# Kernel tuning notes

Hardware: AMD Instinct MI355X
Metric: run time of the kernel (lower is better)

Reference implementation:

```python
import jax, jax.numpy as jnp
import numpy as np
from jax import lax

B, N, T, H = 128, 2, 256, 128  # batch, inc_nodes, seq_len, lstm hidden


def setup_inputs() -> dict:
    key = jax.random.key(0)
    ks = jax.random.split(key, 20)
    r = lambda i, shape, s: (jax.random.normal(ks[i], shape) * s).astype(jnp.float32)
    return {
        "x": r(0, (B, N, T), 1.0),
        "h0": r(1, (N, 4, B, H), 1.0),   # (node, layer*D+dir, B, H), torch.randn init states
        "c0": r(2, (N, 4, B, H), 1.0),
        "w_ih0": r(3, (N, 2, 4 * H, 1), 0.05),
        "w_hh0": r(4, (N, 2, 4 * H, H), 0.05),
        "b0": r(5, (N, 2, 4 * H), 0.05),
        "w_ih1": r(6, (N, 2, 4 * H, 2 * H), 0.05),
        "w_hh1": r(7, (N, 2, 4 * H, H), 0.05),
        "b1": r(8, (N, 2, 4 * H), 0.05),
        "w_fc0": r(9, (N * 2 * H, 256), 0.05), "b_fc0": r(10, (256,), 0.05),
        "ln0_a": r(11, (256,), 1.0), "ln0_b": r(12, (256,), 1.0),
        "w_fc1": r(13, (256, 256), 0.05), "b_fc1": r(14, (256,), 0.05),
        "ln1_a": r(15, (256,), 1.0), "ln1_b": r(16, (256,), 1.0),
        "w_fc2": r(17, (256, 64), 0.05), "b_fc2": r(18, (64,), 0.05),
    }


def _lstm_dir(xp, h0, c0, w_hh):
    # xp: [T, B, 4H] precomputed input projections + bias; returns [T, B, H]
    def step(hc, xt):
        h, c = hc
        g = xt + h @ w_hh.T
        i, f, gg, o = jnp.split(g, 4, axis=-1)  # torch gate order i,f,g,o
        c = jax.nn.sigmoid(f) * c + jax.nn.sigmoid(i) * jnp.tanh(gg)
        h = jax.nn.sigmoid(o) * jnp.tanh(c)
        return (h, c), h
    _, hs = lax.scan(step, (h0, c0), xp)
    return hs


def _bidir(x, h0, c0, w_ih, w_hh, b):
    # x: [B,T,Din]; h0,c0: [2,B,H]; w_ih: [2,4H,Din]; w_hh: [2,4H,H]; b: [2,4H]
    xp_f = jnp.moveaxis(x @ w_ih[0].T + b[0], 1, 0)            # [T,B,4H]
    hf = _lstm_dir(xp_f, h0[0], c0[0], w_hh[0])
    xp_b = jnp.moveaxis(x[:, ::-1] @ w_ih[1].T + b[1], 1, 0)
    hb = _lstm_dir(xp_b, h0[1], c0[1], w_hh[1])[::-1]
    return jnp.moveaxis(jnp.concatenate([hf, hb], axis=-1), 0, 1)  # [B,T,2H]


def _node(xn, h0n, c0n, wi0, wh0, bb0, wi1, wh1, bb1):
    # xn: [B,T,1]; h0n/c0n: [4,B,H] laid out (l0f, l0b, l1f, l1b)
    y = _bidir(xn, h0n[0:2], c0n[0:2], wi0, wh0, bb0)
    y = _bidir(y, h0n[2:4], c0n[2:4], wi1, wh1, bb1)
    return y[:, -1]  # last timestep, [B,2H]


def _layernorm(x, a, b, eps=1e-6):
    mu = jnp.mean(x, axis=-1, keepdims=True)
    std = jnp.std(x, axis=-1, keepdims=True, ddof=1) + eps  # torch.std is unbiased
    return (x - mu) / std * a + b


def reference(x, h0, c0, w_ih0, w_hh0, b0, w_ih1, w_hh1, b1,
              w_fc0, b_fc0, ln0_a, ln0_b, w_fc1, b_fc1, ln1_a, ln1_b, w_fc2, b_fc2):
    bsz = x.shape[0]
    xs = jnp.moveaxis(x, 1, 0)[..., None]  # [N,B,T,1]
    outs = jax.vmap(_node)(xs, h0, c0, w_ih0, w_hh0, b0, w_ih1, w_hh1, b1)  # [N,B,2H]
    t = jnp.moveaxis(outs, 0, 1).reshape(bsz, -1)  # hstack over nodes -> [B, N*2H]
    t = t @ w_fc0 + b_fc0
    t = jax.nn.relu(t + _layernorm(t, ln0_a, ln0_b))
    t = t @ w_fc1 + b_fc1
    t = jax.nn.relu(t + _layernorm(t, ln1_a, ln1_b))
    t = t @ w_fc2 + b_fc2
    return t.reshape(-1, 1, t.shape[-1])  # [B,1,out_dim]
```

## Files before the change

kernel.cpp:

```cpp
#include <hip/hip_runtime.h>
#include <hip/hip_fp16.h>

#define T_SEQ 256

typedef _Float16 half8 __attribute__((ext_vector_type(8)));
typedef float float4v __attribute__((ext_vector_type(4)));

__device__ __forceinline__ float fexp2(float x) { return __builtin_amdgcn_exp2f(x); }
__device__ __forceinline__ float frcp(float x) { return __builtin_amdgcn_rcpf(x); }
__device__ __forceinline__ float sigf(float x) { return frcp(1.f + fexp2(-1.4426950408889634f * x)); }
__device__ __forceinline__ float tanhf_(float x) { return 1.f - 2.f * frcp(1.f + fexp2(2.8853900817779268f * x)); }

__device__ __forceinline__ void gload_lds16(const void* g, void* l) {
    __builtin_amdgcn_global_load_lds((const __attribute__((address_space(1))) void*)g,
                                     (__attribute__((address_space(3))) void*)l, 16, 0, 0);
}

__device__ __forceinline__ void relaxed_barrier() {
    __builtin_amdgcn_sched_barrier(0);
    asm volatile("s_waitcnt lgkmcnt(0)" ::: "memory");
    __builtin_amdgcn_s_barrier();
    asm volatile("" ::: "memory");
    __builtin_amdgcn_sched_barrier(0);
}
__device__ __forceinline__ void vm_barrier() {
    __builtin_amdgcn_sched_barrier(0);
    asm volatile("s_waitcnt vmcnt(0) lgkmcnt(0)" ::: "memory");
    __builtin_amdgcn_s_barrier();
    asm volatile("" ::: "memory");
    __builtin_amdgcn_sched_barrier(0);
}

__global__ __launch_bounds__(512, 1) void lstm_l0(
    const float* __restrict__ x, const float* __restrict__ h0,
    const float* __restrict__ c0, const float* __restrict__ wih0,
    const float* __restrict__ whh0, const float* __restrict__ b0,
    _Float16* __restrict__ y0f) {
    const int wg = blockIdx.x;
    const int chain = wg >> 3, n = chain >> 1, d = chain & 1;
    const int bg = wg & 7, bbase = bg * 16;
    const int tid = threadIdx.x;
    const int wave = tid >> 6, lane = tid & 63, lrow = lane & 15, lgrp = lane >> 4;

    __shared__ __align__(16) float xsT[T_SEQ][16];
    __shared__ __align__(16) _Float16 hfrag[2][4][64][8];

    {
        int r = tid >> 5, ck = tid & 31;
        const float* xr = &x[((bbase + r) * 2 + n) * T_SEQ + ck * 8];
        float4v v0 = *(const float4v*)xr, v1 = *(const float4v*)(xr + 4);
#pragma unroll
        for (int i = 0; i < 4; ++i) { xsT[ck * 8 + i][r] = v0[i]; xsT[ck * 8 + 4 + i][r] = v1[i]; }
    }
    const int sidx = n * 4 + d;
    for (int idx = tid; idx < 256; idx += 512) {
        int kk = idx >> 6, l = idx & 63;
        int b = bbase + (l & 15), k0 = kk * 32 + (l >> 4) * 8;
        const float4v* s4 = (const float4v*)&h0[((size_t)(sidx * 128 + b)) * 128 + k0];
        float4v v0 = s4[0], v1 = s4[1];
        _Float16* dp = &hfrag[0][kk][l][0];
#pragma unroll
        for (int j = 0; j < 4; ++j) { dp[j] = (_Float16)v0[j]; dp[4 + j] = (_Float16)v1[j]; }
    }
    float wi[4], bi[4];
    half8 wf[4][4];
#pragma unroll
    for (int p = 0; p < 4; ++p) {
        int g = (wave + 8 * p) * 16 + lrow;
        wi[p] = wih0[chain * 512 + g];
        bi[p] = b0[chain * 512 + g];
        const float* sg = &whh0[(size_t)(chain * 512 + g) * 128];
#pragma unroll
        for (int kk = 0; kk < 4; ++kk) {
            const float4v* s4 = (const float4v*)&sg[kk * 32 + lgrp * 8];
            float4v v0 = s4[0], v1 = s4[1];
            half8 h;
#pragma unroll
            for (int j = 0; j < 4; ++j) { h[j] = (_Float16)v0[j]; h[4 + j] = (_Float16)v1[j]; }
            wf[p][kk] = h;
        }
    }
    const int hc = wave * 16 + lrow;
    float creg[4];
#pragma unroll
    for (int jj = 0; jj < 4; ++jj)
        creg[jj] = c0[((size_t)(sidx * 128 + bbase + 4 * lgrp + jj)) * 128 + hc];
    __syncthreads();

    const int kkw = hc >> 5, lsub = (hc >> 3) & 3, jd = hc & 7;

    for (int t = 0; t < T_SEQ; ++t) {
        const int cur = t & 1, nxt = cur ^ 1;
        const int tx = d ? (T_SEQ - 1 - t) : t;
        half8 a[4];
#pragma unroll
        for (int kk = 0; kk < 4; ++kk) a[kk] = *(const half8*)&hfrag[cur][kk][lane][0];
        if (t > 0 && tid < 256) {
            const int txp = d ? (T_SEQ - t) : (t - 1);
            half8 v = ((const half8*)&hfrag[cur][0][0][0])[tid];
            half8* dst = (half8*)&y0f[((size_t)(n * 256 + txp) * 8 + bg) * 4096 + d * 2048];
            dst[tid] = v;
        }
        float4v xv = *(const float4v*)&xsT[tx][4 * lgrp];
        float4v acc[4];
#pragma unroll
        for (int p = 0; p < 4; ++p) {
#pragma unroll
            for (int jj = 0; jj < 4; ++jj) acc[p][jj] = fmaf(xv[jj], wi[p], bi[p]);
        }
#pragma unroll
        for (int kk = 0; kk < 4; ++kk)
#pragma unroll
            for (int p = 0; p < 4; ++p)
                acc[p] = __builtin_amdgcn_mfma_f32_16x16x32_f16(a[kk], wf[p][kk], acc[p], 0, 0, 0);
#pragma unroll
        for (int jj = 0; jj < 4; ++jj) {
            float ig = sigf(acc[0][jj]), fg = sigf(acc[1][jj]);
            float gg = tanhf_(acc[2][jj]), og = sigf(acc[3][jj]);
            float c = fmaf(fg, creg[jj], ig * gg);
            creg[jj] = c;
            hfrag[nxt][kkw][16 * lsub + 4 * lgrp + jj][jd] = (_Float16)(og * tanhf_(c));
        }
        relaxed_barrier();
    }
    if (tid < 256) {
        const int txl = d ? 0 : (T_SEQ - 1);
        half8 v = ((const half8*)&hfrag[0][0][0][0])[tid];
        half8* dst = (half8*)&y0f[((size_t)(n * 256 + txl) * 8 + bg) * 4096 + d * 2048];
        dst[tid] = v;
    }
}

__global__ __launch_bounds__(512, 1) void lstm_l1(
    const float* __restrict__ h0, const float* __restrict__ c0,
    const float* __restrict__ wih1, const float* __restrict__ whh1,
    const float* __restrict__ b1, const _Float16* __restrict__ y0f,
    float* __restrict__ lo) {
    const int wg = blockIdx.x;
    const int chain = wg >> 3, n = chain >> 1, d = chain & 1;
    const int bg = wg & 7, bbase = bg * 16;
    const int tid = threadIdx.x;
    const int wave = tid >> 6, lane = tid & 63, lrow = lane & 15, lgrp = lane >> 4;

    __shared__ __align__(16) _Float16 ybuf[2][4096];
    __shared__ __align__(16) _Float16 hfrag[2][4][64][8];

    const int sidx = n * 4 + 2 + d;
    for (int idx = tid; idx < 256; idx += 512) {
        int kk = idx >> 6, l = idx & 63;
        int b = bbase + (l & 15), k0 = kk * 32 + (l >> 4) * 8;
        const float4v* s4 = (const float4v*)&h0[((size_t)(sidx * 128 + b)) * 128 + k0];
        float4v v0 = s4[0], v1 = s4[1];
        _Float16* dp = &hfrag[0][kk][l][0];
#pragma unroll
        for (int j = 0; j < 4; ++j) { dp[j] = (_Float16)v0[j]; dp[4 + j] = (_Float16)v1[j]; }
    }
    float bi[4];
    half8 wih[4][8];
    half8 wf[4][4];
#pragma unroll
    for (int p = 0; p < 4; ++p) {
        int g = (wave + 8 * p) * 16 + lrow;
        bi[p] = b1[chain * 512 + g];
        const float* sg = &wih1[(size_t)(chain * 512 + g) * 256];
#pragma unroll
        for (int kk = 0; kk < 8; ++kk) {
            const float4v* s4 = (const float4v*)&sg[kk * 32 + lgrp * 8];
            float4v v0 = s4[0], v1 = s4[1];
            half8 h;
#pragma unroll
            for (int j = 0; j < 4; ++j) { h[j] = (_Float16)v0[j]; h[4 + j] = (_Float16)v1[j]; }
            wih[p][kk] = h;
        }
        const float* sh = &whh1[(size_t)(chain * 512 + g) * 128];
#pragma unroll
        for (int kk = 0; kk < 4; ++kk) {
            const float4v* s4 = (const float4v*)&sh[kk * 32 + lgrp * 8];
            float4v v0 = s4[0], v1 = s4[1];
            half8 h;
#pragma unroll
            for (int j = 0; j < 4; ++j) { h[j] = (_Float16)v0[j]; h[4 + j] = (_Float16)v1[j]; }
            wf[p][kk] = h;
        }
    }
    const int hc = wave * 16 + lrow;
    float creg[4];
#pragma unroll
    for (int jj = 0; jj < 4; ++jj)
        creg[jj] = c0[((size_t)(sidx * 128 + bbase + 4 * lgrp + jj)) * 128 + hc];

    const int nsteps = d ? 1 : T_SEQ;
    const int t0 = d ? (T_SEQ - 1) : 0;
    gload_lds16(&y0f[(((size_t)n * 256 + t0) * 8 + bg) * 4096 + (size_t)tid * 8],
                &ybuf[0][wave * 512]);
    asm volatile("s_waitcnt vmcnt(0)" ::: "memory");
    __syncthreads();

    const int kkw = hc >> 5, lsub = (hc >> 3) & 3, jd = hc & 7;

    for (int t = 0; t < nsteps; ++t) {
        const int cur = t & 1, nxt = cur ^ 1;
        if (t + 1 < nsteps)
            gload_lds16(&y0f[(((size_t)n * 256 + (t + 1)) * 8 + bg) * 4096 + (size_t)tid * 8],
                        &ybuf[nxt][wave * 512]);
        half8 ay[8], ah[4];
#pragma unroll
        for (int kk = 0; kk < 8; ++kk) ay[kk] = *(const half8*)&ybuf[cur][kk * 512 + lane * 8];
#pragma unroll
        for (int kk = 0; kk < 4; ++kk) ah[kk] = *(const half8*)&hfrag[cur][kk][lane][0];
        float4v acc[4];
#pragma unroll
        for (int p = 0; p < 4; ++p) acc[p] = (float4v){bi[p], bi[p], bi[p], bi[p]};
#pragma unroll
        for (int kk = 0; kk < 8; ++kk)
#pragma unroll
            for (int p = 0; p < 4; ++p)
                acc[p] = __builtin_amdgcn_mfma_f32_16x16x32_f16(ay[kk], wih[p][kk], acc[p], 0, 0, 0);
#pragma unroll
        for (int kk = 0; kk < 4; ++kk)
#pragma unroll
            for (int p = 0; p < 4; ++p)
                acc[p] = __builtin_amdgcn_mfma_f32_16x16x32_f16(ah[kk], wf[p][kk], acc[p], 0, 0, 0);
        float hout[4];
#pragma unroll
        for (int jj = 0; jj < 4; ++jj) {
            float ig = sigf(acc[0][jj]), fg = sigf(acc[1][jj]);
            float gg = tanhf_(acc[2][jj]), og = sigf(acc[3][jj]);
            float c = fmaf(fg, creg[jj], ig * gg);
            creg[jj] = c;
            hout[jj] = og * tanhf_(c);
        }
#pragma unroll
        for (int jj = 0; jj < 4; ++jj)
            hfrag[nxt][kkw][16 * lsub + 4 * lgrp + jj][jd] = (_Float16)hout[jj];
        if (t == nsteps - 1) {
#pragma unroll
            for (int jj = 0; jj < 4; ++jj)
                lo[(size_t)(bbase + 4 * lgrp + jj) * 512 + n * 256 + d * 128 + hc] = hout[jj];
        }
        vm_barrier();
    }
}

__global__ __launch_bounds__(256) void head_k(
    const float* __restrict__ lo,
    const float* __restrict__ w0, const float* __restrict__ bb0,
    const float* __restrict__ a0, const float* __restrict__ g0,
    const float* __restrict__ w1, const float* __restrict__ bb1,
    const float* __restrict__ a1, const float* __restrict__ g1,
    const float* __restrict__ w2, const float* __restrict__ bb2,
    float* __restrict__ out) {
    const int b = blockIdx.x, j = threadIdx.x;
    const int lane = j & 63, wid = j >> 6;
    __shared__ float row[512];
    __shared__ float buf[256];
    __shared__ float redA[4], redB[4];

    row[j] = lo[b * 512 + j];
    row[256 + j] = lo[b * 512 + 256 + j];
    __syncthreads();

    float s = bb0[j];
#pragma unroll 8
    for (int k = 0; k < 512; ++k) s = fmaf(row[k], w0[k * 256 + j], s);
    float v = s, v2 = s * s;
#pragma unroll
    for (int off = 32; off; off >>= 1) { v += __shfl_xor(v, off); v2 += __shfl_xor(v2, off); }
    if (lane == 0) { redA[wid] = v; redB[wid] = v2; }
    __syncthreads();
    float S = redA[0] + redA[1] + redA[2] + redA[3];
    float SS = redB[0] + redB[1] + redB[2] + redB[3];
    float mu = S * (1.f / 256.f);
    float var = (SS - S * mu) * (1.f / 255.f);
    float stdv = sqrtf(var) + 1e-6f;
    float t0 = fmaxf(s + (s - mu) / stdv * a0[j] + g0[j], 0.f);
    buf[j] = t0;
    __syncthreads();

    float s1 = bb1[j];
#pragma unroll 8
    for (int k = 0; k < 256; ++k) s1 = fmaf(buf[k], w1[k * 256 + j], s1);
    v = s1; v2 = s1 * s1;
#pragma unroll
    for (int off = 32; off; off >>= 1) { v += __shfl_xor(v, off); v2 += __shfl_xor(v2, off); }
    if (lane == 0) { redA[wid] = v; redB[wid] = v2; }
    __syncthreads();
    S = redA[0] + redA[1] + redA[2] + redA[3];
    SS = redB[0] + redB[1] + redB[2] + redB[3];
    mu = S * (1.f / 256.f);
    var = (SS - S * mu) * (1.f / 255.f);
    stdv = sqrtf(var) + 1e-6f;
    float t1 = fmaxf(s1 + (s1 - mu) / stdv * a1[j] + g1[j], 0.f);
    __syncthreads();
    buf[j] = t1;
    __syncthreads();

    if (j < 64) {
        float s2 = bb2[j];
#pragma unroll 8
        for (int k = 0; k < 256; ++k) s2 = fmaf(buf[k], w2[k * 64 + j], s2);
        out[b * 64 + j] = s2;
    }
}

extern "C" void kernel_launch(void* const* d_in, const int* in_sizes, int n_in,
                              void* d_out, int out_size, void* d_ws, size_t ws_size,
                              hipStream_t stream) {
    const float* x    = (const float*)d_in[0];
    const float* h0   = (const float*)d_in[1];
    const float* c0   = (const float*)d_in[2];
    const float* wih0 = (const float*)d_in[3];
    const float* whh0 = (const float*)d_in[4];
    const float* bb0  = (const float*)d_in[5];
    const float* wih1 = (const float*)d_in[6];
    const float* whh1 = (const float*)d_in[7];
    const float* bb1  = (const float*)d_in[8];
    const float* wfc0 = (const float*)d_in[9];
    const float* bfc0 = (const float*)d_in[10];
    const float* ln0a = (const float*)d_in[11];
    const float* ln0b = (const float*)d_in[12];
    const float* wfc1 = (const float*)d_in[13];
    const float* bfc1 = (const float*)d_in[14];
    const float* ln1a = (const float*)d_in[15];
    const float* ln1b = (const float*)d_in[16];
    const float* wfc2 = (const float*)d_in[17];
    const float* bfc2 = (const float*)d_in[18];

    char* ws = (char*)d_ws;
    _Float16* y0f = (_Float16*)ws;
    float*    lo  = (float*)(ws + (size_t)33554432);

    lstm_l0<<<dim3(32), dim3(512), 0, stream>>>(x, h0, c0, wih0, whh0, bb0, y0f);
    lstm_l1<<<dim3(32), dim3(512), 0, stream>>>(h0, c0, wih1, whh1, bb1, y0f, lo);
    head_k<<<dim3(128), dim3(256), 0, stream>>>(lo, wfc0, bfc0, ln0a, ln0b,
                                                wfc1, bfc1, ln1a, ln1b, wfc2, bfc2,
                                                (float*)d_out);
}
```

Measured before the change: 755.9 us.

## Split LSTM batch across four times more workgroups with 4-row tiles

Each LSTM chain now runs on 32 workgroups of 4 batch rows instead of 8 workgroups of 16 rows, so 128 workgroups are launched in place of 32 and more compute units stay busy on the serial recurrence. MFMA tiles keep a 16-row shape, but only 4 rows are real and the rest are zero-padded. Gate values are redistributed through an LDS bounce buffer so each lane handles one element, and the MFMA accumulation is split into independent chains to shorten dependency latency. Each step pays for a wasted share of MFMA work and an extra LDS round trip.

Result: slower. 910.9 us (+20.5%).

```diff
diff --git a/kernel.cpp b/kernel.cpp
--- a/kernel.cpp
+++ b/kernel.cpp
@@ -5,6 +5,7 @@
 
 typedef _Float16 half8 __attribute__((ext_vector_type(8)));
 typedef float float4v __attribute__((ext_vector_type(4)));
+typedef float float2v __attribute__((ext_vector_type(2)));
 
 __device__ __forceinline__ float fexp2(float x) { return __builtin_amdgcn_exp2f(x); }
 __device__ __forceinline__ float frcp(float x) { return __builtin_amdgcn_rcpf(x); }
@@ -37,28 +38,29 @@
     const float* __restrict__ whh0, const float* __restrict__ b0,
     _Float16* __restrict__ y0f) {
     const int wg = blockIdx.x;
-    const int chain = wg >> 3, n = chain >> 1, d = chain & 1;
-    const int bg = wg & 7, bbase = bg * 16;
+    const int chain = wg >> 5, n = chain >> 1, d = chain & 1;
+    const int bg4 = wg & 31, bg16 = bg4 >> 2, ro0 = (bg4 & 3) * 4, bbase = bg4 * 4;
     const int tid = threadIdx.x;
     const int wave = tid >> 6, lane = tid & 63, lrow = lane & 15, lgrp = lane >> 4;
 
-    __shared__ __align__(16) float xsT[T_SEQ][16];
+    __shared__ __align__(16) float xsT[T_SEQ][4];
     __shared__ __align__(16) _Float16 hfrag[2][4][64][8];
-
+    __shared__ __align__(16) float bounce[8][4][4][64];
+
+    ((float4v*)hfrag)[tid] = (float4v){0.f, 0.f, 0.f, 0.f};
     {
-        int r = tid >> 5, ck = tid & 31;
-        const float* xr = &x[((bbase + r) * 2 + n) * T_SEQ + ck * 8];
-        float4v v0 = *(const float4v*)xr, v1 = *(const float4v*)(xr + 4);
-#pragma unroll
-        for (int i = 0; i < 4; ++i) { xsT[ck * 8 + i][r] = v0[i]; xsT[ck * 8 + 4 + i][r] = v1[i]; }
-    }
+        int r = tid >> 7, c2 = (tid & 127) * 2;
+        float2v v = *(const float2v*)&x[((bbase + r) * 2 + n) * T_SEQ + c2];
+        xsT[c2][r] = v[0];
+        xsT[c2 + 1][r] = v[1];
+    }
+    __syncthreads();
     const int sidx = n * 4 + d;
-    for (int idx = tid; idx < 256; idx += 512) {
-        int kk = idx >> 6, l = idx & 63;
-        int b = bbase + (l & 15), k0 = kk * 32 + (l >> 4) * 8;
-        const float4v* s4 = (const float4v*)&h0[((size_t)(sidx * 128 + b)) * 128 + k0];
+    if (tid < 64) {
+        int kk = tid >> 4, q = (tid >> 2) & 3, r = tid & 3;
+        const float4v* s4 = (const float4v*)&h0[((size_t)(sidx * 128 + bbase + r)) * 128 + kk * 32 + q * 8];
         float4v v0 = s4[0], v1 = s4[1];
-        _Float16* dp = &hfrag[0][kk][l][0];
+        _Float16* dp = &hfrag[0][kk][16 * q + r][0];
 #pragma unroll
         for (int j = 0; j < 4; ++j) { dp[j] = (_Float16)v0[j]; dp[4 + j] = (_Float16)v1[j]; }
     }
@@ -81,13 +83,11 @@
         }
     }
     const int hc = wave * 16 + lrow;
-    float creg[4];
-#pragma unroll
-    for (int jj = 0; jj < 4; ++jj)
-        creg[jj] = c0[((size_t)(sidx * 128 + bbase + 4 * lgrp + jj)) * 128 + hc];
-    __syncthreads();
-
-    const int kkw = hc >> 5, lsub = (hc >> 3) & 3, jd = hc & 7;
+    float creg = c0[((size_t)(sidx * 128 + bbase + lgrp)) * 128 + hc];
+    __syncthreads();
+
+    const int kkw = hc >> 5, lw = 16 * ((hc >> 3) & 3), jw = hc & 7;
+    const int wb = wave * 8 + lane;
 
     for (int t = 0; t < T_SEQ; ++t) {
         const int cur = t & 1, nxt = cur ^ 1;
@@ -95,39 +95,49 @@
         half8 a[4];
 #pragma unroll
         for (int kk = 0; kk < 4; ++kk) a[kk] = *(const half8*)&hfrag[cur][kk][lane][0];
-        if (t > 0 && tid < 256) {
+        if (t > 0 && lane < 8) {
             const int txp = d ? (T_SEQ - t) : (t - 1);
-            half8 v = ((const half8*)&hfrag[cur][0][0][0])[tid];
-            half8* dst = (half8*)&y0f[((size_t)(n * 256 + txp) * 8 + bg) * 4096 + d * 2048];
-            dst[tid] = v;
-        }
-        float4v xv = *(const float4v*)&xsT[tx][4 * lgrp];
-        float4v acc[4];
-#pragma unroll
-        for (int p = 0; p < 4; ++p) {
-#pragma unroll
-            for (int jj = 0; jj < 4; ++jj) acc[p][jj] = fmaf(xv[jj], wi[p], bi[p]);
-        }
-#pragma unroll
-        for (int kk = 0; kk < 4; ++kk)
-#pragma unroll
-            for (int p = 0; p < 4; ++p)
-                acc[p] = __builtin_amdgcn_mfma_f32_16x16x32_f16(a[kk], wf[p][kk], acc[p], 0, 0, 0);
-#pragma unroll
-        for (int jj = 0; jj < 4; ++jj) {
-            float ig = sigf(acc[0][jj]), fg = sigf(acc[1][jj]);
-            float gg = tanhf_(acc[2][jj]), og = sigf(acc[3][jj]);
-            float c = fmaf(fg, creg[jj], ig * gg);
-            creg[jj] = c;
-            hfrag[nxt][kkw][16 * lsub + 4 * lgrp + jj][jd] = (_Float16)(og * tanhf_(c));
-        }
+            const int kkh = wb >> 4, q = (wb >> 2) & 3, ro = wb & 3;
+            half8 v = *(const half8*)&hfrag[cur][kkh][16 * q + ro][0];
+            *(half8*)&y0f[((size_t)(n * 256 + txp) * 8 + bg16) * 4096 +
+                          (size_t)((d * 4 + kkh) * 64 + 16 * q + ro0 + ro) * 8] = v;
+        }
+        float4v xv = *(const float4v*)&xsT[tx][0];
+        float4v accA[4], accB[4];
+#pragma unroll
+        for (int p = 0; p < 4; ++p) {
+#pragma unroll
+            for (int jj = 0; jj < 4; ++jj) accA[p][jj] = fmaf(xv[jj], wi[p], bi[p]);
+            accB[p] = (float4v){0.f, 0.f, 0.f, 0.f};
+        }
+#pragma unroll
+        for (int p = 0; p < 4; ++p) {
+            accA[p] = __builtin_amdgcn_mfma_f32_16x16x32_f16(a[0], wf[p][0], accA[p], 0, 0, 0);
+            accA[p] = __builtin_amdgcn_mfma_f32_16x16x32_f16(a[1], wf[p][1], accA[p], 0, 0, 0);
+            accB[p] = __builtin_amdgcn_mfma_f32_16x16x32_f16(a[2], wf[p][2], accB[p], 0, 0, 0);
+            accB[p] = __builtin_amdgcn_mfma_f32_16x16x32_f16(a[3], wf[p][3], accB[p], 0, 0, 0);
+        }
+#pragma unroll
+        for (int p = 0; p < 4; ++p) {
+            float4v g = accA[p] + accB[p];
+            *(float4v*)&bounce[wave][p][lgrp][lrow * 4] = g;
+        }
+        float gate[4];
+#pragma unroll
+        for (int p = 0; p < 4; ++p) gate[p] = bounce[wave][p][0][lrow * 4 + lgrp];
+        float ig = sigf(gate[0]), fg = sigf(gate[1]);
+        float gg = tanhf_(gate[2]), og = sigf(gate[3]);
+        creg = fmaf(fg, creg, ig * gg);
+        float ho = og * tanhf_(creg);
+        hfrag[nxt][kkw][lgrp + lw][jw] = (_Float16)ho;
         relaxed_barrier();
     }
-    if (tid < 256) {
+    if (lane < 8) {
         const int txl = d ? 0 : (T_SEQ - 1);
-        half8 v = ((const half8*)&hfrag[0][0][0][0])[tid];
-        half8* dst = (half8*)&y0f[((size_t)(n * 256 + txl) * 8 + bg) * 4096 + d * 2048];
-        dst[tid] = v;
+        const int kkh = wb >> 4, q = (wb >> 2) & 3, ro = wb & 3;
+        half8 v = *(const half8*)&hfrag[0][kkh][16 * q + ro][0];
+        *(half8*)&y0f[((size_t)(n * 256 + txl) * 8 + bg16) * 4096 +
+                      (size_t)((d * 4 + kkh) * 64 + 16 * q + ro0 + ro) * 8] = v;
     }
 }
 
@@ -137,21 +147,23 @@
     const float* __restrict__ b1, const _Float16* __restrict__ y0f,
     float* __restrict__ lo) {
     const int wg = blockIdx.x;
-    const int chain = wg >> 3, n = chain >> 1, d = chain & 1;
-    const int bg = wg & 7, bbase = bg * 16;
+    const int chain = wg >> 5, n = chain >> 1, d = chain & 1;
+    const int bg4 = wg & 31, bg16 = bg4 >> 2, ro0 = (bg4 & 3) * 4, bbase = bg4 * 4;
     const int tid = threadIdx.x;
     const int wave = tid >> 6, lane = tid & 63, lrow = lane & 15, lgrp = lane >> 4;
 
     __shared__ __align__(16) _Float16 ybuf[2][4096];
     __shared__ __align__(16) _Float16 hfrag[2][4][64][8];
-
+    __shared__ __align__(16) float bounce[8][4][4][64];
+
+    ((float4v*)hfrag)[tid] = (float4v){0.f, 0.f, 0.f, 0.f};
+    __syncthreads();
     const int sidx = n * 4 + 2 + d;
-    for (int idx = tid; idx < 256; idx += 512) {
-        int kk = idx >> 6, l = idx & 63;
-        int b = bbase + (l & 15), k0 = kk * 32 + (l >> 4) * 8;
-        const float4v* s4 = (const float4v*)&h0[((size_t)(sidx * 128 + b)) * 128 + k0];
+    if (tid < 64) {
+        int kk = tid >> 4, q = (tid >> 2) & 3, r = tid & 3;
+        const float4v* s4 = (const float4v*)&h0[((size_t)(sidx * 128 + bbase + r)) * 128 + kk * 32 + q * 8];
         float4v v0 = s4[0], v1 = s4[1];
-        _Float16* dp = &hfrag[0][kk][l][0];
+        _Float16* dp = &hfrag[0][kk][16 * q + ro0 + r][0];
 #pragma unroll
         for (int j = 0; j < 4; ++j) { dp[j] = (_Float16)v0[j]; dp[4 + j] = (_Float16)v1[j]; }
     }
@@ -184,60 +196,65 @@
         }
     }
     const int hc = wave * 16 + lrow;
-    float creg[4];
-#pragma unroll
-    for (int jj = 0; jj < 4; ++jj)
-        creg[jj] = c0[((size_t)(sidx * 128 + bbase + 4 * lgrp + jj)) * 128 + hc];
+    float creg = c0[((size_t)(sidx * 128 + bbase + lgrp)) * 128 + hc];
 
     const int nsteps = d ? 1 : T_SEQ;
     const int t0 = d ? (T_SEQ - 1) : 0;
-    gload_lds16(&y0f[(((size_t)n * 256 + t0) * 8 + bg) * 4096 + (size_t)tid * 8],
+    gload_lds16(&y0f[((size_t)(n * 256 + t0) * 8 + bg16) * 4096 + (size_t)tid * 8],
                 &ybuf[0][wave * 512]);
     asm volatile("s_waitcnt vmcnt(0)" ::: "memory");
     __syncthreads();
 
-    const int kkw = hc >> 5, lsub = (hc >> 3) & 3, jd = hc & 7;
+    const int kkw = hc >> 5, lw = 16 * ((hc >> 3) & 3), jw = hc & 7;
+    const int srcg = bg4 & 3;
 
     for (int t = 0; t < nsteps; ++t) {
         const int cur = t & 1, nxt = cur ^ 1;
         if (t + 1 < nsteps)
-            gload_lds16(&y0f[(((size_t)n * 256 + (t + 1)) * 8 + bg) * 4096 + (size_t)tid * 8],
+            gload_lds16(&y0f[((size_t)(n * 256 + (t + 1)) * 8 + bg16) * 4096 + (size_t)tid * 8],
                         &ybuf[nxt][wave * 512]);
         half8 ay[8], ah[4];
 #pragma unroll
         for (int kk = 0; kk < 8; ++kk) ay[kk] = *(const half8*)&ybuf[cur][kk * 512 + lane * 8];
 #pragma unroll
         for (int kk = 0; kk < 4; ++kk) ah[kk] = *(const half8*)&hfrag[cur][kk][lane][0];
-        float4v acc[4];
-#pragma unroll
-        for (int p = 0; p < 4; ++p) acc[p] = (float4v){bi[p], bi[p], bi[p], bi[p]};
-#pragma unroll
-        for (int kk = 0; kk < 8; ++kk)
-#pragma unroll
-            for (int p = 0; p < 4; ++p)
-                acc[p] = __builtin_amdgcn_mfma_f32_16x16x32_f16(ay[kk], wih[p][kk], acc[p], 0, 0, 0);
-#pragma unroll
-        for (int kk = 0; kk < 4; ++kk)
-#pragma unroll
-            for (int p = 0; p < 4; ++p)
-                acc[p] = __builtin_amdgcn_mfma_f32_16x16x32_f16(ah[kk], wf[p][kk], acc[p], 0, 0, 0);
-        float hout[4];
-#pragma unroll
-        for (int jj = 0; jj < 4; ++jj) {
-            float ig = sigf(acc[0][jj]), fg = sigf(acc[1][jj]);
-            float gg = tanhf_(acc[2][jj]), og = sigf(acc[3][jj]);
-            float c = fmaf(fg, creg[jj], ig * gg);
-            creg[jj] = c;
-            hout[jj] = og * tanhf_(c);
-        }
-#pragma unroll
-        for (int jj = 0; jj < 4; ++jj)
-            hfrag[nxt][kkw][16 * lsub + 4 * lgrp + jj][jd] = (_Float16)hout[jj];
-        if (t == nsteps - 1) {
-#pragma unroll
-            for (int jj = 0; jj < 4; ++jj)
-                lo[(size_t)(bbase + 4 * lgrp + jj) * 512 + n * 256 + d * 128 + hc] = hout[jj];
-        }
+        float4v accA[4], accB[4], accC[4];
+#pragma unroll
+        for (int p = 0; p < 4; ++p) {
+            accA[p] = (float4v){bi[p], bi[p], bi[p], bi[p]};
+            accB[p] = (float4v){0.f, 0.f, 0.f, 0.f};
+            accC[p] = (float4v){0.f, 0.f, 0.f, 0.f};
+        }
+#pragma unroll
+        for (int p = 0; p < 4; ++p) {
+            accA[p] = __builtin_amdgcn_mfma_f32_16x16x32_f16(ay[0], wih[p][0], accA[p], 0, 0, 0);
+            accA[p] = __builtin_amdgcn_mfma_f32_16x16x32_f16(ay[1], wih[p][1], accA[p], 0, 0, 0);
+            accA[p] = __builtin_amdgcn_mfma_f32_16x16x32_f16(ay[2], wih[p][2], accA[p], 0, 0, 0);
+            accA[p] = __builtin_amdgcn_mfma_f32_16x16x32_f16(ay[3], wih[p][3], accA[p], 0, 0, 0);
+            accB[p] = __builtin_amdgcn_mfma_f32_16x16x32_f16(ay[4], wih[p][4], accB[p], 0, 0, 0);
+            accB[p] = __builtin_amdgcn_mfma_f32_16x16x32_f16(ay[5], wih[p][5], accB[p], 0, 0, 0);
+            accB[p] = __builtin_amdgcn_mfma_f32_16x16x32_f16(ay[6], wih[p][6], accB[p], 0, 0, 0);
+            accB[p] = __builtin_amdgcn_mfma_f32_16x16x32_f16(ay[7], wih[p][7], accB[p], 0, 0, 0);
+            accC[p] = __builtin_amdgcn_mfma_f32_16x16x32_f16(ah[0], wf[p][0], accC[p], 0, 0, 0);
+            accC[p] = __builtin_amdgcn_mfma_f32_16x16x32_f16(ah[1], wf[p][1], accC[p], 0, 0, 0);
+            accC[p] = __builtin_amdgcn_mfma_f32_16x16x32_f16(ah[2], wf[p][2], accC[p], 0, 0, 0);
+            accC[p] = __builtin_amdgcn_mfma_f32_16x16x32_f16(ah[3], wf[p][3], accC[p], 0, 0, 0);
+        }
+#pragma unroll
+        for (int p = 0; p < 4; ++p) {
+            float4v g = accA[p] + accB[p] + accC[p];
+            *(float4v*)&bounce[wave][p][lgrp][lrow * 4] = g;
+        }
+        float gate[4];
+#pragma unroll
+        for (int p = 0; p < 4; ++p) gate[p] = bounce[wave][p][srcg][lrow * 4 + lgrp];
+        float ig = sigf(gate[0]), fg = sigf(gate[1]);
+        float gg = tanhf_(gate[2]), og = sigf(gate[3]);
+        creg = fmaf(fg, creg, ig * gg);
+        float ho = og * tanhf_(creg);
+        hfrag[nxt][kkw][ro0 + lgrp + lw][jw] = (_Float16)ho;
+        if (t == nsteps - 1)
+            lo[(size_t)(bbase + lgrp) * 512 + n * 256 + d * 128 + hc] = ho;
         vm_barrier();
     }
 }
@@ -330,8 +347,8 @@
     _Float16* y0f = (_Float16*)ws;
     float*    lo  = (float*)(ws + (size_t)33554432);
 
-    lstm_l0<<<dim3(32), dim3(512), 0, stream>>>(x, h0, c0, wih0, whh0, bb0, y0f);
-    lstm_l1<<<dim3(32), dim3(512), 0, stream>>>(h0, c0, wih1, whh1, bb1, y0f, lo);
+    lstm_l0<<<dim3(128), dim3(512), 0, stream>>>(x, h0, c0, wih0, whh0, bb0, y0f);
+    lstm_l1<<<dim3(128), dim3(512), 0, stream>>>(h0, c0, wih1, whh1, bb1, y0f, lo);
     head_k<<<dim3(128), dim3(256), 0, stream>>>(lo, wfc0, bfc0, ln0a, ln0b,
                                                 wfc1, bfc1, ln1a, ln1b, wfc2, bfc2,
                                                 (float*)d_out);
```

## Software-pipeline layer-1 input projection and fuse LSTM gate math

Applied to the files above, without the earlier changes.

The layer-1 kernel now computes the input-projection MFMAs for step t+1 after the recurrent MFMAs of step t, so they are off the recurrent critical path. This uses a triple-buffered LDS prefetch of y0 two steps ahead. Gate math is merged into a single function that shares reciprocals (one rcp for the i·g product, one for o·tanh(c)), with clamping to avoid overflow. Layer 0 splits its MFMA accumulation into two independent chains to shorten the dependency, and all 512 threads now write 8-byte stores instead of 256 threads writing 16 bytes. The cost is extra LDS and registers, plus slightly different numerics from the combined reciprocals.

Result: slower. 818.9 us (+8.3%).

```diff
diff --git a/kernel.cpp b/kernel.cpp
--- a/kernel.cpp
+++ b/kernel.cpp
@@ -5,11 +5,30 @@
 
 typedef _Float16 half8 __attribute__((ext_vector_type(8)));
 typedef float float4v __attribute__((ext_vector_type(4)));
+typedef unsigned long long u64;
 
 __device__ __forceinline__ float fexp2(float x) { return __builtin_amdgcn_exp2f(x); }
 __device__ __forceinline__ float frcp(float x) { return __builtin_amdgcn_rcpf(x); }
-__device__ __forceinline__ float sigf(float x) { return frcp(1.f + fexp2(-1.4426950408889634f * x)); }
-__device__ __forceinline__ float tanhf_(float x) { return 1.f - 2.f * frcp(1.f + fexp2(2.8853900817779268f * x)); }
+
+__device__ __forceinline__ float lstm_gate(float gi, float gf, float gg, float go, float& c) {
+    const float K1 = -1.4426950408889634f;
+    const float K2 = 2.8853900817779268f;
+    gi = __builtin_amdgcn_fmed3f(gi, -30.f, 30.f);
+    gf = __builtin_amdgcn_fmed3f(gf, -30.f, 30.f);
+    gg = __builtin_amdgcn_fmed3f(gg, -30.f, 30.f);
+    go = __builtin_amdgcn_fmed3f(go, -30.f, 30.f);
+    float F2 = fexp2(K1 * gf);
+    float A2 = fexp2(K1 * gi);
+    float G2 = fexp2(K2 * gg);
+    float O2 = fexp2(K1 * go);
+    float rf  = frcp(1.f + F2);
+    float rag = frcp((1.f + A2) * (1.f + G2));
+    c = c * rf + (G2 - 1.f) * rag;
+    float cc = __builtin_amdgcn_fmed3f(c, -20.f, 20.f);
+    float C2 = fexp2(K2 * cc);
+    float roc = frcp((1.f + O2) * (1.f + C2));
+    return (C2 - 1.f) * roc;
+}
 
 __device__ __forceinline__ void gload_lds16(const void* g, void* l) {
     __builtin_amdgcn_global_load_lds((const __attribute__((address_space(1))) void*)g,
@@ -87,7 +106,7 @@
         creg[jj] = c0[((size_t)(sidx * 128 + bbase + 4 * lgrp + jj)) * 128 + hc];
     __syncthreads();
 
-    const int kkw = hc >> 5, lsub = (hc >> 3) & 3, jd = hc & 7;
+    const int kkw = hc >> 5, lw = 16 * ((hc >> 3) & 3), jw = hc & 7;
 
     for (int t = 0; t < T_SEQ; ++t) {
         const int cur = t & 1, nxt = cur ^ 1;
@@ -95,39 +114,41 @@
         half8 a[4];
 #pragma unroll
         for (int kk = 0; kk < 4; ++kk) a[kk] = *(const half8*)&hfrag[cur][kk][lane][0];
-        if (t > 0 && tid < 256) {
+        if (t > 0) {
             const int txp = d ? (T_SEQ - t) : (t - 1);
-            half8 v = ((const half8*)&hfrag[cur][0][0][0])[tid];
-            half8* dst = (half8*)&y0f[((size_t)(n * 256 + txp) * 8 + bg) * 4096 + d * 2048];
-            dst[tid] = v;
+            u64 v = ((const u64*)&hfrag[cur][0][0][0])[tid];
+            ((u64*)&y0f[((size_t)(n * 256 + txp) * 8 + bg) * 4096 + d * 2048])[tid] = v;
         }
         float4v xv = *(const float4v*)&xsT[tx][4 * lgrp];
-        float4v acc[4];
+        float4v accA[4], accB[4];
 #pragma unroll
         for (int p = 0; p < 4; ++p) {
 #pragma unroll
-            for (int jj = 0; jj < 4; ++jj) acc[p][jj] = fmaf(xv[jj], wi[p], bi[p]);
-        }
-#pragma unroll
-        for (int kk = 0; kk < 4; ++kk)
-#pragma unroll
-            for (int p = 0; p < 4; ++p)
-                acc[p] = __builtin_amdgcn_mfma_f32_16x16x32_f16(a[kk], wf[p][kk], acc[p], 0, 0, 0);
+            for (int jj = 0; jj < 4; ++jj) accA[p][jj] = fmaf(xv[jj], wi[p], bi[p]);
+            accB[p] = (float4v){0.f, 0.f, 0.f, 0.f};
+        }
+#pragma unroll
+        for (int p = 0; p < 4; ++p) {
+            accA[p] = __builtin_amdgcn_mfma_f32_16x16x32_f16(a[0], wf[p][0], accA[p], 0, 0, 0);
+            accA[p] = __builtin_amdgcn_mfma_f32_16x16x32_f16(a[1], wf[p][1], accA[p], 0, 0, 0);
+            accB[p] = __builtin_amdgcn_mfma_f32_16x16x32_f16(a[2], wf[p][2], accB[p], 0, 0, 0);
+            accB[p] = __builtin_amdgcn_mfma_f32_16x16x32_f16(a[3], wf[p][3], accB[p], 0, 0, 0);
+        }
 #pragma unroll
         for (int jj = 0; jj < 4; ++jj) {
-            float ig = sigf(acc[0][jj]), fg = sigf(acc[1][jj]);
-            float gg = tanhf_(acc[2][jj]), og = sigf(acc[3][jj]);
-            float c = fmaf(fg, creg[jj], ig * gg);
-            creg[jj] = c;
-            hfrag[nxt][kkw][16 * lsub + 4 * lgrp + jj][jd] = (_Float16)(og * tanhf_(c));
+            float gi = accA[0][jj] + accB[0][jj];
+            float gf = accA[1][jj] + accB[1][jj];
+            float gg = accA[2][jj] + accB[2][jj];
+            float go = accA[3][jj] + accB[3][jj];
+            float ho = lstm_gate(gi, gf, gg, go, creg[jj]);
+            hfrag[nxt][kkw][lw + 4 * lgrp + jj][jw] = (_Float16)ho;
         }
         relaxed_barrier();
     }
-    if (tid < 256) {
+    {
         const int txl = d ? 0 : (T_SEQ - 1);
-        half8 v = ((const half8*)&hfrag[0][0][0][0])[tid];
-        half8* dst = (half8*)&y0f[((size_t)(n * 256 + txl) * 8 + bg) * 4096 + d * 2048];
-        dst[tid] = v;
+        u64 v = ((const u64*)&hfrag[0][0][0][0])[tid];
+        ((u64*)&y0f[((size_t)(n * 256 + txl) * 8 + bg) * 4096 + d * 2048])[tid] = v;
     }
 }
 
@@ -142,7 +163,7 @@
     const int tid = threadIdx.x;
     const int wave = tid >> 6, lane = tid & 63, lrow = lane & 15, lgrp = lane >> 4;
 
-    __shared__ __align__(16) _Float16 ybuf[2][4096];
+    __shared__ __align__(16) _Float16 ybuf[3][4096];
     __shared__ __align__(16) _Float16 hfrag[2][4][64][8];
 
     const int sidx = n * 4 + 2 + d;
@@ -191,53 +212,75 @@
 
     const int nsteps = d ? 1 : T_SEQ;
     const int t0 = d ? (T_SEQ - 1) : 0;
-    gload_lds16(&y0f[(((size_t)n * 256 + t0) * 8 + bg) * 4096 + (size_t)tid * 8],
+    gload_lds16(&y0f[((size_t)(n * 256 + t0) * 8 + bg) * 4096 + (size_t)tid * 8],
                 &ybuf[0][wave * 512]);
+    if (nsteps > 1)
+        gload_lds16(&y0f[((size_t)(n * 256 + t0 + 1) * 8 + bg) * 4096 + (size_t)tid * 8],
+                    &ybuf[1][wave * 512]);
     asm volatile("s_waitcnt vmcnt(0)" ::: "memory");
     __syncthreads();
 
-    const int kkw = hc >> 5, lsub = (hc >> 3) & 3, jd = hc & 7;
+    float4v accY[4];
+#pragma unroll
+    for (int p = 0; p < 4; ++p) accY[p] = (float4v){bi[p], bi[p], bi[p], bi[p]};
+#pragma unroll
+    for (int kk = 0; kk < 8; ++kk) {
+        half8 ay = *(const half8*)&ybuf[0][kk * 512 + lane * 8];
+#pragma unroll
+        for (int p = 0; p < 4; ++p)
+            accY[p] = __builtin_amdgcn_mfma_f32_16x16x32_f16(ay, wih[p][kk], accY[p], 0, 0, 0);
+    }
+
+    const int kkw = hc >> 5, lw = 16 * ((hc >> 3) & 3), jw = hc & 7;
+    int sRd = 1, sFl = 2, sOld = 0;
 
     for (int t = 0; t < nsteps; ++t) {
         const int cur = t & 1, nxt = cur ^ 1;
-        if (t + 1 < nsteps)
-            gload_lds16(&y0f[(((size_t)n * 256 + (t + 1)) * 8 + bg) * 4096 + (size_t)tid * 8],
-                        &ybuf[nxt][wave * 512]);
-        half8 ay[8], ah[4];
-#pragma unroll
-        for (int kk = 0; kk < 8; ++kk) ay[kk] = *(const half8*)&ybuf[cur][kk * 512 + lane * 8];
-#pragma unroll
-        for (int kk = 0; kk < 4; ++kk) ah[kk] = *(const half8*)&hfrag[cur][kk][lane][0];
+        const int tf = (t + 2 < nsteps) ? (t + 2) : (nsteps - 1);
+        gload_lds16(&y0f[((size_t)(n * 256 + t0 + tf) * 8 + bg) * 4096 + (size_t)tid * 8],
+                    &ybuf[sFl][wave * 512]);
         float4v acc[4];
-#pragma unroll
-        for (int p = 0; p < 4; ++p) acc[p] = (float4v){bi[p], bi[p], bi[p], bi[p]};
-#pragma unroll
-        for (int kk = 0; kk < 8; ++kk)
-#pragma unroll
-            for (int p = 0; p < 4; ++p)
-                acc[p] = __builtin_amdgcn_mfma_f32_16x16x32_f16(ay[kk], wih[p][kk], acc[p], 0, 0, 0);
-#pragma unroll
-        for (int kk = 0; kk < 4; ++kk)
-#pragma unroll
-            for (int p = 0; p < 4; ++p)
-                acc[p] = __builtin_amdgcn_mfma_f32_16x16x32_f16(ah[kk], wf[p][kk], acc[p], 0, 0, 0);
+        {
+            half8 a0 = *(const half8*)&hfrag[cur][0][lane][0];
+            half8 a1 = *(const half8*)&hfrag[cur][1][lane][0];
+#pragma unroll
+            for (int p = 0; p < 4; ++p)
+                acc[p] = __builtin_amdgcn_mfma_f32_16x16x32_f16(a0, wf[p][0], accY[p], 0, 0, 0);
+#pragma unroll
+            for (int p = 0; p < 4; ++p)
+                acc[p] = __builtin_amdgcn_mfma_f32_16x16x32_f16(a1, wf[p][1], acc[p], 0, 0, 0);
+            half8 a2 = *(const half8*)&hfrag[cur][2][lane][0];
+            half8 a3 = *(const half8*)&hfrag[cur][3][lane][0];
+#pragma unroll
+            for (int p = 0; p < 4; ++p)
+                acc[p] = __builtin_amdgcn_mfma_f32_16x16x32_f16(a2, wf[p][2], acc[p], 0, 0, 0);
+#pragma unroll
+            for (int p = 0; p < 4; ++p)
+                acc[p] = __builtin_amdgcn_mfma_f32_16x16x32_f16(a3, wf[p][3], acc[p], 0, 0, 0);
+        }
+        const _Float16* yb = &ybuf[sRd][lane * 8];
+#pragma unroll
+        for (int p = 0; p < 4; ++p) accY[p] = (float4v){bi[p], bi[p], bi[p], bi[p]};
+#pragma unroll
+        for (int kk = 0; kk < 8; ++kk) {
+            half8 ay = *(const half8*)&yb[kk * 512];
+#pragma unroll
+            for (int p = 0; p < 4; ++p)
+                accY[p] = __builtin_amdgcn_mfma_f32_16x16x32_f16(ay, wih[p][kk], accY[p], 0, 0, 0);
+        }
         float hout[4];
 #pragma unroll
-        for (int jj = 0; jj < 4; ++jj) {
-            float ig = sigf(acc[0][jj]), fg = sigf(acc[1][jj]);
-            float gg = tanhf_(acc[2][jj]), og = sigf(acc[3][jj]);
-            float c = fmaf(fg, creg[jj], ig * gg);
-            creg[jj] = c;
-            hout[jj] = og * tanhf_(c);
-        }
-#pragma unroll
         for (int jj = 0; jj < 4; ++jj)
-            hfrag[nxt][kkw][16 * lsub + 4 * lgrp + jj][jd] = (_Float16)hout[jj];
+            hout[jj] = lstm_gate(acc[0][jj], acc[1][jj], acc[2][jj], acc[3][jj], creg[jj]);
+#pragma unroll
+        for (int jj = 0; jj < 4; ++jj)
+            hfrag[nxt][kkw][lw + 4 * lgrp + jj][jw] = (_Float16)hout[jj];
         if (t == nsteps - 1) {
 #pragma unroll
             for (int jj = 0; jj < 4; ++jj)
                 lo[(size_t)(bbase + 4 * lgrp + jj) * 512 + n * 256 + d * 128 + hc] = hout[jj];
         }
+        int tmp = sOld; sOld = sRd; sRd = sFl; sFl = tmp;
         vm_barrier();
     }
 }
```
